# Kernel tuning notes

Hardware: AMD Instinct MI355X
Metric: run time of the kernel (lower is better)

Reference implementation:

```python
import jax, jax.numpy as jnp
import numpy as np

B, L, D, H = 2, 2048, 1024, 16
DH = D // H  # 64


def setup_inputs() -> dict:
    key = jax.random.key(0)
    ks = jax.random.split(key, 9)
    s = 1.0 / np.sqrt(D)
    x = jax.random.normal(ks[0], (B, L, D), dtype=jnp.float32)
    # per-head projection weights stacked on leading head axis (torch Linear: y = x W^T + b)
    Wq = jax.random.normal(ks[1], (H, D, DH), dtype=jnp.float32) * s
    bq = jax.random.normal(ks[2], (H, DH), dtype=jnp.float32) * s
    Wk = jax.random.normal(ks[3], (H, D, DH), dtype=jnp.float32) * s
    bk = jax.random.normal(ks[4], (H, DH), dtype=jnp.float32) * s
    Wv = jax.random.normal(ks[5], (H, D, DH), dtype=jnp.float32) * s
    bv = jax.random.normal(ks[6], (H, DH), dtype=jnp.float32) * s
    WO = jax.random.normal(ks[7], (D, D), dtype=jnp.float32) * s  # torch layout [out, in]
    bO = jax.random.normal(ks[8], (D,), dtype=jnp.float32) * s
    return {"x": x, "Wq": Wq, "bq": bq, "Wk": Wk, "bk": bk,
            "Wv": Wv, "bv": bv, "WO": WO, "bO": bO}


def reference(x, Wq, bq, Wk, bk, Wv, bv, WO, bO):
    # Q,K,V: [B,H,L,DH]
    Q = jnp.einsum('bld,hdk->bhlk', x, Wq) + bq[None, :, None, :]
    K = jnp.einsum('bld,hdk->bhlk', x, Wk) + bk[None, :, None, :]
    V = jnp.einsum('bld,hdk->bhlk', x, Wv) + bv[None, :, None, :]
    scale = 1.0 / jnp.sqrt(jnp.asarray(DH, dtype=x.dtype))
    att = jnp.einsum('bhik,bhjk->bhij', Q, K) * scale  # [B,H,Lq,Lk]
    # NOTE: original softmaxes over dim=1 of [B,Lq,Lk] -> the QUERY axis (axis=2 here)
    att = jax.nn.softmax(att, axis=2)
    # dropout is identity in eval/reference mode
    out = jnp.einsum('bhij,bhjk->bhik', att, V)  # [B,H,L,DH]
    out = out.transpose(0, 2, 1, 3).reshape(B, L, D)  # concat heads on feature axis
    return jnp.einsum('bld,ed->ble', out, WO) + bO
```

## Files before the change

### kernel.cpp

```cpp
#include <hip/hip_runtime.h>
#include <math.h>

#define NB 2
#define NL 2048
#define ND 1024
#define NH 16
#define NDH 64
static constexpr float SCALE = 0.125f;

typedef short          bhalf8 __attribute__((ext_vector_type(8)));
typedef unsigned short ush8   __attribute__((ext_vector_type(8)));
typedef unsigned short ush4   __attribute__((ext_vector_type(4)));
typedef float          f32x4  __attribute__((ext_vector_type(4)));

#define MFMA_BF16(a, b, c) __builtin_amdgcn_mfma_f32_16x16x32_bf16(a, b, c, 0, 0, 0)

__device__ __forceinline__ unsigned short f2bf(float f) {
    unsigned u = __float_as_uint(f);
    u += 0x7FFF + ((u >> 16) & 1);
    return (unsigned short)(u >> 16);
}
__device__ __forceinline__ float bf2f(unsigned short s) {
    return __uint_as_float((unsigned)s << 16);
}
__device__ __forceinline__ unsigned pack_bf16(float lo, float hi) {
    unsigned a = __float_as_uint(lo) + 0x8000u;
    unsigned b = __float_as_uint(hi) + 0x8000u;
    return __builtin_amdgcn_perm(b, a, 0x07060302u);
}

__global__ __launch_bounds__(256) void k_cvt(
    const float* __restrict__ x, const float* __restrict__ WO,
    unsigned short* __restrict__ xb, unsigned short* __restrict__ wob)
{
    size_t u = (size_t)blockIdx.x * 256 + threadIdx.x;
    const float* src; unsigned short* dst; size_t off;
    if (u < 524288) { src = x;  dst = xb;  off = u * 8; }
    else            { src = WO; dst = wob; off = (u - 524288) * 8; }
    float4 a = *(const float4*)(src + off);
    float4 b = *(const float4*)(src + off + 4);
    uint4 o;
    o.x = pack_bf16(a.x, a.y); o.y = pack_bf16(a.z, a.w);
    o.z = pack_bf16(b.x, b.y); o.w = pack_bf16(b.z, b.w);
    *(uint4*)(dst + off) = o;
}

__global__ __launch_bounds__(256) void k_cvt_wt(
    const float* __restrict__ Wq, const float* __restrict__ Wk,
    const float* __restrict__ Wv, unsigned short* __restrict__ Wtb)
{
    __shared__ unsigned short T[64][72];
    const int d0  = blockIdx.x * 64;
    const int qkv = blockIdx.y >> 4;
    const int h   = blockIdx.y & 15;
    const float* W = (qkv == 0 ? Wq : (qkv == 1 ? Wk : Wv)) + (size_t)h * (ND * NDH);
    const int t = threadIdx.x;
#pragma unroll
    for (int p = 0; p < 4; ++p) {
        int u  = t + p * 256;
        int dr = u >> 4;
        int c4 = (u & 15) * 4;
        float4 v = *(const float4*)(W + (size_t)(d0 + dr) * NDH + c4);
        T[c4 + 0][dr] = f2bf(v.x);
        T[c4 + 1][dr] = f2bf(v.y);
        T[c4 + 2][dr] = f2bf(v.z);
        T[c4 + 3][dr] = f2bf(v.w);
    }
    __syncthreads();
    unsigned short* outp = Wtb + (size_t)(qkv * NH + h) * NDH * ND;
#pragma unroll
    for (int p = 0; p < 2; ++p) {
        int u  = t + p * 256;
        int dh = u >> 3;
        int sg = (u & 7) * 8;
        *(ush8*)(outp + (size_t)dh * ND + d0 + sg) = *(ush8*)&T[dh][sg];
    }
}

__global__ __launch_bounds__(256, 2) void k_qkv_mfma(
    const unsigned short* __restrict__ xb, const unsigned short* __restrict__ Wtb,
    const float* __restrict__ bq, const float* __restrict__ bk,
    const float* __restrict__ bv,
    unsigned short* __restrict__ Qb, unsigned short* __restrict__ Kb,
    unsigned short* __restrict__ Vtb)
{
    __shared__ unsigned short LB[2 * 128 * 64];
    unsigned short* As = LB;
    unsigned short* Bs = LB + 128 * 64;

    const int mt = blockIdx.x;
    const int nt = blockIdx.y;
    const int qkv = nt >> 3;
    const int t = threadIdx.x, w = t >> 6, lane = t & 63;
    const int lr = lane & 15, lg = lane >> 4;
    const int wm = (w >> 1) * 64, wn = (w & 1) * 64;
    const int swz = (lr & 7) << 3;

    f32x4 acc[4][4] = {};

    for (int k0 = 0; k0 < ND; k0 += 64) {
        __syncthreads();
#pragma unroll
        for (int p = 0; p < 4; ++p) {
            int u = t + p * 256;
            int r = u >> 3, sg = (u & 7) * 8;
            int sc = sg ^ ((r & 7) << 3);
            *(ush8*)&As[r * 64 + sc] = *(const ush8*)(xb  + (size_t)(mt * 128 + r) * ND + k0 + sg);
            *(ush8*)&Bs[r * 64 + sc] = *(const ush8*)(Wtb + (size_t)(nt * 128 + r) * ND + k0 + sg);
        }
        __syncthreads();

        bhalf8 av[4][2], bw[4][2];
#pragma unroll
        for (int f = 0; f < 4; ++f)
#pragma unroll
            for (int ks = 0; ks < 2; ++ks) {
                int c = (ks * 32 + lg * 8) ^ swz;
                av[f][ks] = *(const bhalf8*)&As[(wm + f * 16 + lr) * 64 + c];
                bw[f][ks] = *(const bhalf8*)&Bs[(wn + f * 16 + lr) * 64 + c];
            }
#pragma unroll
        for (int mf = 0; mf < 4; ++mf)
#pragma unroll
            for (int nf = 0; nf < 4; ++nf) {
                acc[mf][nf] = MFMA_BF16(av[mf][0], bw[nf][0], acc[mf][nf]);
                acc[mf][nf] = MFMA_BF16(av[mf][1], bw[nf][1], acc[mf][nf]);
            }
    }

    const float* bias = (qkv == 0 ? bq : (qkv == 1 ? bk : bv));
    const int nb = (nt & 7) * 128;
    float bi[4];
#pragma unroll
    for (int nf = 0; nf < 4; ++nf) bi[nf] = bias[nb + wn + nf * 16 + lr];

    __syncthreads();
    unsigned short* TS = LB;

    if (qkv < 2) {
#pragma unroll
        for (int mf = 0; mf < 4; ++mf)
#pragma unroll
            for (int nf = 0; nf < 4; ++nf)
#pragma unroll
                for (int r = 0; r < 4; ++r) {
                    int m = wm + mf * 16 + lg * 4 + r;
                    int n = (wn + nf * 16 + lr) ^ ((m & 7) << 3);
                    TS[m * 128 + n] = f2bf(acc[mf][nf][r] + bi[nf]);
                }
        __syncthreads();
        unsigned short* outp = (qkv == 0 ? Qb : Kb);
#pragma unroll
        for (int p = 0; p < 8; ++p) {
            int u = t + p * 256;
            int r = u >> 4, sg = (u & 15) * 8;
            ush8 v = *(const ush8*)&TS[r * 128 + (sg ^ ((r & 7) << 3))];
            int m = mt * 128 + r;
            int b = m >> 11, l = m & (NL - 1);
            int n = nb + sg;
            int h = n >> 6, dh = n & 63;
            *(ush8*)(outp + ((size_t)(b * NH + h) * NL + l) * NDH + dh) = v;
        }
    } else {
#pragma unroll
        for (int mf = 0; mf < 4; ++mf)
#pragma unroll
            for (int nf = 0; nf < 4; ++nf) {
                int n = wn + nf * 16 + lr;
                int mc = (wm + mf * 16 + lg * 4) ^ ((n & 7) << 3);
                ush4 pk;
#pragma unroll
                for (int r = 0; r < 4; ++r) pk[r] = f2bf(acc[mf][nf][r] + bi[nf]);
                *(ush4*)&TS[n * 128 + mc] = pk;
            }
        __syncthreads();
#pragma unroll
        for (int p = 0; p < 8; ++p) {
            int u = t + p * 256;
            int r = u >> 4, sg = (u & 15) * 8;
            ush8 v = *(const ush8*)&TS[r * 128 + (sg ^ ((r & 7) << 3))];
            int n = nb + r;
            int h = n >> 6, dh = n & 63;
            int m0 = mt * 128 + sg;
            int b = m0 >> 11, l0 = m0 & (NL - 1);
            *(ush8*)(Vtb + ((size_t)(b * NH + h) * NDH + dh) * NL + l0) = v;
        }
    }
}

__global__ __launch_bounds__(256, 3) void k_colsum_mfma(
    const unsigned short* __restrict__ Qb, const unsigned short* __restrict__ Kb,
    unsigned short* __restrict__ Vtb)
{
    __shared__ unsigned short Ks[128 * 64];
    __shared__ unsigned short Qs[64 * 64];
    __shared__ float rzbuf[128];

    const int jt = blockIdx.x;
    const int bh = blockIdx.y;
    const unsigned short* Qp = Qb + (size_t)bh * NL * NDH;
    const unsigned short* Kp = Kb + (size_t)bh * NL * NDH;
    const int t = threadIdx.x, w = t >> 6, lane = t & 63;
    const int lr = lane & 15, lg = lane >> 4;
    const int wj = w * 32;
    const int swz = (lr & 7) << 3;

#pragma unroll
    for (int p = 0; p < 4; ++p) {
        int u = t + p * 256;
        int r = u >> 3, sg = (u & 7) * 8;
        *(ush8*)&Ks[r * 64 + (sg ^ ((r & 7) << 3))] =
            *(const ush8*)(Kp + (size_t)(jt * 128 + r) * NDH + sg);
    }

    float zacc[2][4] = {};

    for (int it = 0; it < 32; ++it) {
        __syncthreads();
#pragma unroll
        for (int p = 0; p < 2; ++p) {
            int u = t + p * 256;
            int r = u >> 3, sg = (u & 7) * 8;
            *(ush8*)&Qs[r * 64 + (sg ^ ((r & 7) << 3))] =
                *(const ush8*)(Qp + (size_t)(it * 64 + r) * NDH + sg);
        }
        __syncthreads();

        bhalf8 ka[2][2], qv[4][2];
#pragma unroll
        for (int jf = 0; jf < 2; ++jf)
#pragma unroll
            for (int ks = 0; ks < 2; ++ks)
                ka[jf][ks] = *(const bhalf8*)&Ks[(wj + jf * 16 + lr) * 64 +
                                                ((ks * 32 + lg * 8) ^ swz)];
#pragma unroll
        for (int ii = 0; ii < 4; ++ii)
#pragma unroll
            for (int ks = 0; ks < 2; ++ks)
                qv[ii][ks] = *(const bhalf8*)&Qs[(ii * 16 + lr) * 64 +
                                                ((ks * 32 + lg * 8) ^ swz)];

#pragma unroll
        for (int jf = 0; jf < 2; ++jf)
#pragma unroll
            for (int ii = 0; ii < 4; ++ii) {
                f32x4 s = {};
                s = MFMA_BF16(ka[jf][0], qv[ii][0], s);
                s = MFMA_BF16(ka[jf][1], qv[ii][1], s);
#pragma unroll
                for (int r = 0; r < 4; ++r)
                    zacc[jf][r] += __expf(s[r] * SCALE);
            }
    }

#pragma unroll
    for (int jf = 0; jf < 2; ++jf)
#pragma unroll
        for (int r = 0; r < 4; ++r) {
            float v = zacc[jf][r];
            v += __shfl_xor(v, 1);
            v += __shfl_xor(v, 2);
            v += __shfl_xor(v, 4);
            v += __shfl_xor(v, 8);
            zacc[jf][r] = v;
        }
    if (lr == 0) {
#pragma unroll
        for (int jf = 0; jf < 2; ++jf)
#pragma unroll
            for (int r = 0; r < 4; ++r)
                rzbuf[wj + jf * 16 + lg * 4 + r] = 1.0f / zacc[jf][r];
    }
    __syncthreads();

    unsigned short* Vp = Vtb + (size_t)bh * NDH * NL + jt * 128;
#pragma unroll
    for (int p = 0; p < 4; ++p) {
        int u = t + p * 256;
        int dh = u >> 4, jj = (u & 15) * 8;
        unsigned short* vp = Vp + (size_t)dh * NL + jj;
        ush8 v = *(const ush8*)vp;
        float4 z0 = *(const float4*)&rzbuf[jj];
        float4 z1 = *(const float4*)&rzbuf[jj + 4];
        uint4 o;
        o.x = pack_bf16(bf2f(v[0]) * z0.x, bf2f(v[1]) * z0.y);
        o.y = pack_bf16(bf2f(v[2]) * z0.z, bf2f(v[3]) * z0.w);
        o.z = pack_bf16(bf2f(v[4]) * z1.x, bf2f(v[5]) * z1.y);
        o.w = pack_bf16(bf2f(v[6]) * z1.z, bf2f(v[7]) * z1.w);
        *(uint4*)vp = o;
    }
}

__global__ __launch_bounds__(256, 3) void k_av_mfma(
    const unsigned short* __restrict__ Qb, const unsigned short* __restrict__ Kb,
    const unsigned short* __restrict__ Vtb, unsigned short* __restrict__ AOb)
{
    __shared__ unsigned short Qs[128 * 64];
    __shared__ unsigned short Ks[64 * 64];
    __shared__ unsigned short Vts[64 * 64];
    __shared__ unsigned short Ps[128 * 64];

    const int it = blockIdx.x;
    const int bh = blockIdx.y;
    const int b = bh >> 4, h = bh & 15;
    const unsigned short* Qp = Qb  + (size_t)bh * NL * NDH;
    const unsigned short* Kp = Kb  + (size_t)bh * NL * NDH;
    const unsigned short* Vp = Vtb + (size_t)bh * NDH * NL;

    const int t = threadIdx.x, w = t >> 6, lane = t & 63;
    const int lr = lane & 15, lg = lane >> 4;
    const int wi = w * 32;
    const int swz = (lr & 7) << 3;

#pragma unroll
    for (int p = 0; p < 4; ++p) {
        int u = t + p * 256;
        int r = u >> 3, sg = (u & 7) * 8;
        *(ush8*)&Qs[r * 64 + (sg ^ ((r & 7) << 3))] =
            *(const ush8*)(Qp + (size_t)(it * 128 + r) * NDH + sg);
    }

    f32x4 oacc[2][4] = {};

    for (int jt = 0; jt < 32; ++jt) {
        __syncthreads();
#pragma unroll
        for (int p = 0; p < 2; ++p) {
            int u = t + p * 256;
            int r = u >> 3, sg = (u & 7) * 8;
            int sc = sg ^ ((r & 7) << 3);
            *(ush8*)&Ks[r * 64 + sc]  = *(const ush8*)(Kp + (size_t)(jt * 64 + r) * NDH + sg);
            *(ush8*)&Vts[r * 64 + sc] = *(const ush8*)(Vp + (size_t)r * NL + jt * 64 + sg);
        }
        __syncthreads();

        bhalf8 ka[4][2], qv[2][2];
#pragma unroll
        for (int jf = 0; jf < 4; ++jf)
#pragma unroll
            for (int ks = 0; ks < 2; ++ks)
                ka[jf][ks] = *(const bhalf8*)&Ks[(jf * 16 + lr) * 64 +
                                                ((ks * 32 + lg * 8) ^ swz)];
#pragma unroll
        for (int ii = 0; ii < 2; ++ii)
#pragma unroll
            for (int ks = 0; ks < 2; ++ks)
                qv[ii][ks] = *(const bhalf8*)&Qs[(wi + ii * 16 + lr) * 64 +
                                                ((ks * 32 + lg * 8) ^ swz)];

#pragma unroll
        for (int ii = 0; ii < 2; ++ii)
#pragma unroll
            for (int jf = 0; jf < 4; ++jf) {
                f32x4 s = {};
                s = MFMA_BF16(ka[jf][0], qv[ii][0], s);
                s = MFMA_BF16(ka[jf][1], qv[ii][1], s);
                uint2 pk;
                pk.x = pack_bf16(__expf(s[0] * SCALE), __expf(s[1] * SCALE));
                pk.y = pack_bf16(__expf(s[2] * SCALE), __expf(s[3] * SCALE));
                *(uint2*)&Ps[(wi + ii * 16 + lr) * 64 + ((jf * 16 + lg * 4) ^ swz)] = pk;
            }
        __syncthreads();

        bhalf8 pa[2][2], vb[4][2];
#pragma unroll
        for (int ii = 0; ii < 2; ++ii)
#pragma unroll
            for (int ks = 0; ks < 2; ++ks)
                pa[ii][ks] = *(const bhalf8*)&Ps[(wi + ii * 16 + lr) * 64 +
                                                ((ks * 32 + lg * 8) ^ swz)];
#pragma unroll
        for (int nf = 0; nf < 4; ++nf)
#pragma unroll
            for (int ks = 0; ks < 2; ++ks)
                vb[nf][ks] = *(const bhalf8*)&Vts[(nf * 16 + lr) * 64 +
                                                 ((ks * 32 + lg * 8) ^ swz)];
#pragma unroll
        for (int ii = 0; ii < 2; ++ii)
#pragma unroll
            for (int nf = 0; nf < 4; ++nf) {
                oacc[ii][nf] = MFMA_BF16(pa[ii][0], vb[nf][0], oacc[ii][nf]);
                oacc[ii][nf] = MFMA_BF16(pa[ii][1], vb[nf][1], oacc[ii][nf]);
            }
    }

    __syncthreads();
#pragma unroll
    for (int ii = 0; ii < 2; ++ii)
#pragma unroll
        for (int nf = 0; nf < 4; ++nf)
#pragma unroll
            for (int r = 0; r < 4; ++r) {
                int l  = wi + ii * 16 + lg * 4 + r;
                int dh = (nf * 16 + lr) ^ ((l & 7) << 3);
                Ps[l * 64 + dh] = f2bf(oacc[ii][nf][r]);
            }
    __syncthreads();
#pragma unroll
    for (int p = 0; p < 4; ++p) {
        int u = t + p * 256;
        int r = u >> 3, sg = (u & 7) * 8;
        ush8 v = *(const ush8*)&Ps[r * 64 + (sg ^ ((r & 7) << 3))];
        *(ush8*)(AOb + ((size_t)(b * NL + it * 128 + r)) * ND + h * NDH + sg) = v;
    }
}

__global__ __launch_bounds__(256, 2) void k_oproj_mfma(
    const unsigned short* __restrict__ AOb, const unsigned short* __restrict__ WOb,
    const float* __restrict__ bO, float* __restrict__ y)
{
    __shared__ unsigned short As[128 * 64];
    __shared__ unsigned short Bs[128 * 64];

    const int mt = blockIdx.x;
    const int nt = blockIdx.y;
    const int t = threadIdx.x, w = t >> 6, lane = t & 63;
    const int lr = lane & 15, lg = lane >> 4;
    const int wm = (w >> 1) * 64, wn = (w & 1) * 64;
    const int swz = (lr & 7) << 3;

    f32x4 acc[4][4] = {};

    for (int k0 = 0; k0 < ND; k0 += 64) {
        __syncthreads();
#pragma unroll
        for (int p = 0; p < 4; ++p) {
            int u = t + p * 256;
            int r = u >> 3, sg = (u & 7) * 8;
            int sc = sg ^ ((r & 7) << 3);
            *(ush8*)&As[r * 64 + sc] = *(const ush8*)(AOb + (size_t)(mt * 128 + r) * ND + k0 + sg);
            *(ush8*)&Bs[r * 64 + sc] = *(const ush8*)(WOb + (size_t)(nt * 128 + r) * ND + k0 + sg);
        }
        __syncthreads();

        bhalf8 av[4][2], bw[4][2];
#pragma unroll
        for (int f = 0; f < 4; ++f)
#pragma unroll
            for (int ks = 0; ks < 2; ++ks) {
                int c = (ks * 32 + lg * 8) ^ swz;
                av[f][ks] = *(const bhalf8*)&As[(wm + f * 16 + lr) * 64 + c];
                bw[f][ks] = *(const bhalf8*)&Bs[(wn + f * 16 + lr) * 64 + c];
            }
#pragma unroll
        for (int mf = 0; mf < 4; ++mf)
#pragma unroll
            for (int nf = 0; nf < 4; ++nf) {
                acc[mf][nf] = MFMA_BF16(av[mf][0], bw[nf][0], acc[mf][nf]);
                acc[mf][nf] = MFMA_BF16(av[mf][1], bw[nf][1], acc[mf][nf]);
            }
    }

#pragma unroll
    for (int mf = 0; mf < 4; ++mf)
#pragma unroll
        for (int nf = 0; nf < 4; ++nf) {
            int e = nt * 128 + wn + nf * 16 + lr;
            float bo = bO[e];
#pragma unroll
            for (int r = 0; r < 4; ++r) {
                int m = mt * 128 + wm + mf * 16 + lg * 4 + r;
                y[(size_t)m * ND + e] = acc[mf][nf][r] + bo;
            }
        }
}

extern "C" void kernel_launch(void* const* d_in, const int* in_sizes, int n_in,
                              void* d_out, int out_size, void* d_ws, size_t ws_size,
                              hipStream_t stream)
{
    const float* x  = (const float*)d_in[0];
    const float* Wq = (const float*)d_in[1];
    const float* bq = (const float*)d_in[2];
    const float* Wk = (const float*)d_in[3];
    const float* bk = (const float*)d_in[4];
    const float* Wv = (const float*)d_in[5];
    const float* bv = (const float*)d_in[6];
    const float* WO = (const float*)d_in[7];
    const float* bO = (const float*)d_in[8];
    float* y = (float*)d_out;

    unsigned short* xb  = (unsigned short*)d_ws;
    unsigned short* Wtb = xb  + 4194304;
    unsigned short* WOb = Wtb + 3145728;
    unsigned short* Qb  = WOb + 1048576;
    unsigned short* Kb  = Qb  + 4194304;
    unsigned short* Vtb = Kb  + 4194304;
    unsigned short* AOb = Vtb + 4194304;

    hipLaunchKernelGGL(k_cvt,         dim3(2560),   dim3(256), 0, stream, x, WO, xb, WOb);
    hipLaunchKernelGGL(k_cvt_wt,      dim3(16, 48), dim3(256), 0, stream, Wq, Wk, Wv, Wtb);
    hipLaunchKernelGGL(k_qkv_mfma,    dim3(32, 24), dim3(256), 0, stream,
                       xb, Wtb, bq, bk, bv, Qb, Kb, Vtb);
    hipLaunchKernelGGL(k_colsum_mfma, dim3(16, 32), dim3(256), 0, stream, Qb, Kb, Vtb);
    hipLaunchKernelGGL(k_av_mfma,     dim3(16, 32), dim3(256), 0, stream, Qb, Kb, Vtb, AOb);
    hipLaunchKernelGGL(k_oproj_mfma,  dim3(32, 8),  dim3(256), 0, stream, AOb, WOb, bO, y);
}
```

Measured before the change: 231.8 us.

## Use direct global-to-LDS loads, 512-thread attention blocks, smaller o-proj tiles

Global-to-shared tile staging in the QKV, column-sum, attention and output-projection kernels now uses `global_load_lds` 16-byte DMA loads. The swizzle is applied on the global source address, so data no longer passes through registers. The column-sum and A·V kernels move to 512-thread blocks, giving each wave a single 16-row slice and fewer registers, which should raise occupancy and latency hiding. The output projection uses 64-row M tiles, doubling the grid to fill more CUs, at the cost of less B-tile reuse per block.

After: 215.7 us. 1.07x faster.

```diff
diff --git a/kernel.cpp b/kernel.cpp
--- a/kernel.cpp
+++ b/kernel.cpp
@@ -27,6 +27,12 @@
     unsigned a = __float_as_uint(lo) + 0x8000u;
     unsigned b = __float_as_uint(hi) + 0x8000u;
     return __builtin_amdgcn_perm(b, a, 0x07060302u);
+}
+__device__ __forceinline__ void gload16(const unsigned short* g, unsigned short* l) {
+    __builtin_amdgcn_global_load_lds(
+        (const __attribute__((address_space(1))) unsigned int*)(const void*)g,
+        (__attribute__((address_space(3))) unsigned int*)(void*)l,
+        16, 0, 0);
 }
 
 __global__ __launch_bounds__(256) void k_cvt(
@@ -95,18 +101,19 @@
     const int lr = lane & 15, lg = lane >> 4;
     const int wm = (w >> 1) * 64, wn = (w & 1) * 64;
     const int swz = (lr & 7) << 3;
+    const int rA = lane >> 3, cg = (lane & 7) * 8;
 
     f32x4 acc[4][4] = {};
 
     for (int k0 = 0; k0 < ND; k0 += 64) {
         __syncthreads();
 #pragma unroll
-        for (int p = 0; p < 4; ++p) {
-            int u = t + p * 256;
-            int r = u >> 3, sg = (u & 7) * 8;
-            int sc = sg ^ ((r & 7) << 3);
-            *(ush8*)&As[r * 64 + sc] = *(const ush8*)(xb  + (size_t)(mt * 128 + r) * ND + k0 + sg);
-            *(ush8*)&Bs[r * 64 + sc] = *(const ush8*)(Wtb + (size_t)(nt * 128 + r) * ND + k0 + sg);
+        for (int i = 0; i < 4; ++i) {
+            int c  = w * 4 + i;
+            int r  = c * 8 + rA;
+            int gc = cg ^ ((r & 7) << 3);
+            gload16(xb  + (size_t)(mt * 128 + r) * ND + k0 + gc, &As[c * 512]);
+            gload16(Wtb + (size_t)(nt * 128 + r) * ND + k0 + gc, &Bs[c * 512]);
         }
         __syncthreads();
 
@@ -188,7 +195,7 @@
     }
 }
 
-__global__ __launch_bounds__(256, 3) void k_colsum_mfma(
+__global__ __launch_bounds__(512, 4) void k_colsum_mfma(
     const unsigned short* __restrict__ Qb, const unsigned short* __restrict__ Kb,
     unsigned short* __restrict__ Vtb)
 {
@@ -202,96 +209,81 @@
     const unsigned short* Kp = Kb + (size_t)bh * NL * NDH;
     const int t = threadIdx.x, w = t >> 6, lane = t & 63;
     const int lr = lane & 15, lg = lane >> 4;
-    const int wj = w * 32;
+    const int wj = w * 16;
     const int swz = (lr & 7) << 3;
-
-#pragma unroll
-    for (int p = 0; p < 4; ++p) {
-        int u = t + p * 256;
-        int r = u >> 3, sg = (u & 7) * 8;
-        *(ush8*)&Ks[r * 64 + (sg ^ ((r & 7) << 3))] =
-            *(const ush8*)(Kp + (size_t)(jt * 128 + r) * NDH + sg);
-    }
-
-    float zacc[2][4] = {};
+    const int rA = lane >> 3, cg = (lane & 7) * 8;
+
+#pragma unroll
+    for (int i = 0; i < 2; ++i) {
+        int c  = w * 2 + i;
+        int r  = c * 8 + rA;
+        int gc = cg ^ ((r & 7) << 3);
+        gload16(Kp + (size_t)(jt * 128 + r) * NDH + gc, &Ks[c * 512]);
+    }
+
+    float zacc[4] = {};
 
     for (int it = 0; it < 32; ++it) {
         __syncthreads();
-#pragma unroll
-        for (int p = 0; p < 2; ++p) {
-            int u = t + p * 256;
-            int r = u >> 3, sg = (u & 7) * 8;
-            *(ush8*)&Qs[r * 64 + (sg ^ ((r & 7) << 3))] =
-                *(const ush8*)(Qp + (size_t)(it * 64 + r) * NDH + sg);
-        }
-        __syncthreads();
-
-        bhalf8 ka[2][2], qv[4][2];
-#pragma unroll
-        for (int jf = 0; jf < 2; ++jf)
-#pragma unroll
-            for (int ks = 0; ks < 2; ++ks)
-                ka[jf][ks] = *(const bhalf8*)&Ks[(wj + jf * 16 + lr) * 64 +
-                                                ((ks * 32 + lg * 8) ^ swz)];
-#pragma unroll
-        for (int ii = 0; ii < 4; ++ii)
-#pragma unroll
-            for (int ks = 0; ks < 2; ++ks)
-                qv[ii][ks] = *(const bhalf8*)&Qs[(ii * 16 + lr) * 64 +
-                                                ((ks * 32 + lg * 8) ^ swz)];
-
-#pragma unroll
-        for (int jf = 0; jf < 2; ++jf)
-#pragma unroll
-            for (int ii = 0; ii < 4; ++ii) {
-                f32x4 s = {};
-                s = MFMA_BF16(ka[jf][0], qv[ii][0], s);
-                s = MFMA_BF16(ka[jf][1], qv[ii][1], s);
-#pragma unroll
-                for (int r = 0; r < 4; ++r)
-                    zacc[jf][r] += __expf(s[r] * SCALE);
-            }
-    }
-
-#pragma unroll
-    for (int jf = 0; jf < 2; ++jf)
-#pragma unroll
-        for (int r = 0; r < 4; ++r) {
-            float v = zacc[jf][r];
-            v += __shfl_xor(v, 1);
-            v += __shfl_xor(v, 2);
-            v += __shfl_xor(v, 4);
-            v += __shfl_xor(v, 8);
-            zacc[jf][r] = v;
-        }
-    if (lr == 0) {
-#pragma unroll
-        for (int jf = 0; jf < 2; ++jf)
-#pragma unroll
-            for (int r = 0; r < 4; ++r)
-                rzbuf[wj + jf * 16 + lg * 4 + r] = 1.0f / zacc[jf][r];
+        {
+            int r  = w * 8 + rA;
+            int gc = cg ^ ((r & 7) << 3);
+            gload16(Qp + (size_t)(it * 64 + r) * NDH + gc, &Qs[w * 512]);
+        }
+        __syncthreads();
+
+        bhalf8 ka[2];
+#pragma unroll
+        for (int ks = 0; ks < 2; ++ks)
+            ka[ks] = *(const bhalf8*)&Ks[(wj + lr) * 64 + ((ks * 32 + lg * 8) ^ swz)];
+#pragma unroll
+        for (int ii = 0; ii < 4; ++ii) {
+            bhalf8 q0 = *(const bhalf8*)&Qs[(ii * 16 + lr) * 64 + ((lg * 8) ^ swz)];
+            bhalf8 q1 = *(const bhalf8*)&Qs[(ii * 16 + lr) * 64 + ((32 + lg * 8) ^ swz)];
+            f32x4 s = {};
+            s = MFMA_BF16(ka[0], q0, s);
+            s = MFMA_BF16(ka[1], q1, s);
+#pragma unroll
+            for (int r = 0; r < 4; ++r) zacc[r] += __expf(s[r] * SCALE);
+        }
+    }
+
+#pragma unroll
+    for (int r = 0; r < 4; ++r) {
+        float v = zacc[r];
+        v += __shfl_xor(v, 1);
+        v += __shfl_xor(v, 2);
+        v += __shfl_xor(v, 4);
+        v += __shfl_xor(v, 8);
+        if (lr == 0) rzbuf[wj + lg * 4 + r] = 1.0f / v;
     }
     __syncthreads();
 
     unsigned short* Vp = Vtb + (size_t)bh * NDH * NL + jt * 128;
-#pragma unroll
-    for (int p = 0; p < 4; ++p) {
-        int u = t + p * 256;
-        int dh = u >> 4, jj = (u & 15) * 8;
+    {
+        int dh = t >> 3, jj = (t & 7) * 16;
         unsigned short* vp = Vp + (size_t)dh * NL + jj;
-        ush8 v = *(const ush8*)vp;
+        ush8 v0 = *(const ush8*)vp;
+        ush8 v1 = *(const ush8*)(vp + 8);
         float4 z0 = *(const float4*)&rzbuf[jj];
         float4 z1 = *(const float4*)&rzbuf[jj + 4];
-        uint4 o;
-        o.x = pack_bf16(bf2f(v[0]) * z0.x, bf2f(v[1]) * z0.y);
-        o.y = pack_bf16(bf2f(v[2]) * z0.z, bf2f(v[3]) * z0.w);
-        o.z = pack_bf16(bf2f(v[4]) * z1.x, bf2f(v[5]) * z1.y);
-        o.w = pack_bf16(bf2f(v[6]) * z1.z, bf2f(v[7]) * z1.w);
-        *(uint4*)vp = o;
-    }
-}
-
-__global__ __launch_bounds__(256, 3) void k_av_mfma(
+        float4 z2 = *(const float4*)&rzbuf[jj + 8];
+        float4 z3 = *(const float4*)&rzbuf[jj + 12];
+        uint4 o0, o1;
+        o0.x = pack_bf16(bf2f(v0[0]) * z0.x, bf2f(v0[1]) * z0.y);
+        o0.y = pack_bf16(bf2f(v0[2]) * z0.z, bf2f(v0[3]) * z0.w);
+        o0.z = pack_bf16(bf2f(v0[4]) * z1.x, bf2f(v0[5]) * z1.y);
+        o0.w = pack_bf16(bf2f(v0[6]) * z1.z, bf2f(v0[7]) * z1.w);
+        o1.x = pack_bf16(bf2f(v1[0]) * z2.x, bf2f(v1[1]) * z2.y);
+        o1.y = pack_bf16(bf2f(v1[2]) * z2.z, bf2f(v1[3]) * z2.w);
+        o1.z = pack_bf16(bf2f(v1[4]) * z3.x, bf2f(v1[5]) * z3.y);
+        o1.w = pack_bf16(bf2f(v1[6]) * z3.z, bf2f(v1[7]) * z3.w);
+        *(uint4*)vp = o0;
+        *(uint4*)(vp + 8) = o1;
+    }
+}
+
+__global__ __launch_bounds__(512, 4) void k_av_mfma(
     const unsigned short* __restrict__ Qb, const unsigned short* __restrict__ Kb,
     const unsigned short* __restrict__ Vtb, unsigned short* __restrict__ AOb)
 {
@@ -309,99 +301,78 @@
 
     const int t = threadIdx.x, w = t >> 6, lane = t & 63;
     const int lr = lane & 15, lg = lane >> 4;
-    const int wi = w * 32;
+    const int wi = w * 16;
     const int swz = (lr & 7) << 3;
-
-#pragma unroll
-    for (int p = 0; p < 4; ++p) {
-        int u = t + p * 256;
-        int r = u >> 3, sg = (u & 7) * 8;
-        *(ush8*)&Qs[r * 64 + (sg ^ ((r & 7) << 3))] =
-            *(const ush8*)(Qp + (size_t)(it * 128 + r) * NDH + sg);
-    }
-
-    f32x4 oacc[2][4] = {};
+    const int rA = lane >> 3, cg = (lane & 7) * 8;
+
+#pragma unroll
+    for (int i = 0; i < 2; ++i) {
+        int c  = w * 2 + i;
+        int r  = c * 8 + rA;
+        int gc = cg ^ ((r & 7) << 3);
+        gload16(Qp + (size_t)(it * 128 + r) * NDH + gc, &Qs[c * 512]);
+    }
+
+    f32x4 oacc[4] = {};
 
     for (int jt = 0; jt < 32; ++jt) {
         __syncthreads();
-#pragma unroll
-        for (int p = 0; p < 2; ++p) {
-            int u = t + p * 256;
-            int r = u >> 3, sg = (u & 7) * 8;
-            int sc = sg ^ ((r & 7) << 3);
-            *(ush8*)&Ks[r * 64 + sc]  = *(const ush8*)(Kp + (size_t)(jt * 64 + r) * NDH + sg);
-            *(ush8*)&Vts[r * 64 + sc] = *(const ush8*)(Vp + (size_t)r * NL + jt * 64 + sg);
-        }
-        __syncthreads();
-
-        bhalf8 ka[4][2], qv[2][2];
-#pragma unroll
-        for (int jf = 0; jf < 4; ++jf)
-#pragma unroll
-            for (int ks = 0; ks < 2; ++ks)
-                ka[jf][ks] = *(const bhalf8*)&Ks[(jf * 16 + lr) * 64 +
-                                                ((ks * 32 + lg * 8) ^ swz)];
-#pragma unroll
-        for (int ii = 0; ii < 2; ++ii)
-#pragma unroll
-            for (int ks = 0; ks < 2; ++ks)
-                qv[ii][ks] = *(const bhalf8*)&Qs[(wi + ii * 16 + lr) * 64 +
-                                                ((ks * 32 + lg * 8) ^ swz)];
-
-#pragma unroll
-        for (int ii = 0; ii < 2; ++ii)
-#pragma unroll
-            for (int jf = 0; jf < 4; ++jf) {
-                f32x4 s = {};
-                s = MFMA_BF16(ka[jf][0], qv[ii][0], s);
-                s = MFMA_BF16(ka[jf][1], qv[ii][1], s);
-                uint2 pk;
-                pk.x = pack_bf16(__expf(s[0] * SCALE), __expf(s[1] * SCALE));
-                pk.y = pack_bf16(__expf(s[2] * SCALE), __expf(s[3] * SCALE));
-                *(uint2*)&Ps[(wi + ii * 16 + lr) * 64 + ((jf * 16 + lg * 4) ^ swz)] = pk;
-            }
-        __syncthreads();
-
-        bhalf8 pa[2][2], vb[4][2];
-#pragma unroll
-        for (int ii = 0; ii < 2; ++ii)
-#pragma unroll
-            for (int ks = 0; ks < 2; ++ks)
-                pa[ii][ks] = *(const bhalf8*)&Ps[(wi + ii * 16 + lr) * 64 +
-                                                ((ks * 32 + lg * 8) ^ swz)];
-#pragma unroll
-        for (int nf = 0; nf < 4; ++nf)
-#pragma unroll
-            for (int ks = 0; ks < 2; ++ks)
-                vb[nf][ks] = *(const bhalf8*)&Vts[(nf * 16 + lr) * 64 +
-                                                 ((ks * 32 + lg * 8) ^ swz)];
-#pragma unroll
-        for (int ii = 0; ii < 2; ++ii)
-#pragma unroll
-            for (int nf = 0; nf < 4; ++nf) {
-                oacc[ii][nf] = MFMA_BF16(pa[ii][0], vb[nf][0], oacc[ii][nf]);
-                oacc[ii][nf] = MFMA_BF16(pa[ii][1], vb[nf][1], oacc[ii][nf]);
-            }
+        {
+            int r  = w * 8 + rA;
+            int gc = cg ^ ((r & 7) << 3);
+            gload16(Kp + (size_t)(jt * 64 + r) * NDH + gc, &Ks[w * 512]);
+            gload16(Vp + (size_t)r * NL + jt * 64 + gc,    &Vts[w * 512]);
+        }
+        __syncthreads();
+
+        bhalf8 qa[2];
+#pragma unroll
+        for (int ks = 0; ks < 2; ++ks)
+            qa[ks] = *(const bhalf8*)&Qs[(wi + lr) * 64 + ((ks * 32 + lg * 8) ^ swz)];
+#pragma unroll
+        for (int jf = 0; jf < 4; ++jf) {
+            bhalf8 k0v = *(const bhalf8*)&Ks[(jf * 16 + lr) * 64 + ((lg * 8) ^ swz)];
+            bhalf8 k1v = *(const bhalf8*)&Ks[(jf * 16 + lr) * 64 + ((32 + lg * 8) ^ swz)];
+            f32x4 s = {};
+            s = MFMA_BF16(k0v, qa[0], s);
+            s = MFMA_BF16(k1v, qa[1], s);
+            uint2 pk;
+            pk.x = pack_bf16(__expf(s[0] * SCALE), __expf(s[1] * SCALE));
+            pk.y = pack_bf16(__expf(s[2] * SCALE), __expf(s[3] * SCALE));
+            *(uint2*)&Ps[(wi + lr) * 64 + ((jf * 16 + lg * 4) ^ swz)] = pk;
+        }
+
+        bhalf8 pa[2];
+#pragma unroll
+        for (int ks = 0; ks < 2; ++ks)
+            pa[ks] = *(const bhalf8*)&Ps[(wi + lr) * 64 + ((ks * 32 + lg * 8) ^ swz)];
+#pragma unroll
+        for (int nf = 0; nf < 4; ++nf) {
+            bhalf8 v0 = *(const bhalf8*)&Vts[(nf * 16 + lr) * 64 + ((lg * 8) ^ swz)];
+            bhalf8 v1 = *(const bhalf8*)&Vts[(nf * 16 + lr) * 64 + ((32 + lg * 8) ^ swz)];
+            oacc[nf] = MFMA_BF16(pa[0], v0, oacc[nf]);
+            oacc[nf] = MFMA_BF16(pa[1], v1, oacc[nf]);
+        }
     }
 
     __syncthreads();
 #pragma unroll
-    for (int ii = 0; ii < 2; ++ii)
-#pragma unroll
-        for (int nf = 0; nf < 4; ++nf)
-#pragma unroll
-            for (int r = 0; r < 4; ++r) {
-                int l  = wi + ii * 16 + lg * 4 + r;
-                int dh = (nf * 16 + lr) ^ ((l & 7) << 3);
-                Ps[l * 64 + dh] = f2bf(oacc[ii][nf][r]);
-            }
+    for (int nf = 0; nf < 4; ++nf)
+#pragma unroll
+        for (int r = 0; r < 4; ++r) {
+            int li  = wi + lg * 4 + r;
+            int dhc = (nf * 16 + lr) ^ ((li & 7) << 3);
+            Ps[li * 64 + dhc] = f2bf(oacc[nf][r]);
+        }
     __syncthreads();
-#pragma unroll
-    for (int p = 0; p < 4; ++p) {
-        int u = t + p * 256;
-        int r = u >> 3, sg = (u & 7) * 8;
-        ush8 v = *(const ush8*)&Ps[r * 64 + (sg ^ ((r & 7) << 3))];
-        *(ush8*)(AOb + ((size_t)(b * NL + it * 128 + r)) * ND + h * NDH + sg) = v;
+    {
+        int r = t >> 2, sgq = (t & 3) * 16;
+        int sz2 = (r & 7) << 3;
+        ush8 v0 = *(const ush8*)&Ps[r * 64 + (sgq ^ sz2)];
+        ush8 v1 = *(const ush8*)&Ps[r * 64 + ((sgq + 8) ^ sz2)];
+        unsigned short* op = AOb + ((size_t)(b * NL + it * 128 + r)) * ND + h * NDH + sgq;
+        *(ush8*)op = v0;
+        *(ush8*)(op + 8) = v1;
     }
 }
 
@@ -409,57 +380,65 @@
     const unsigned short* __restrict__ AOb, const unsigned short* __restrict__ WOb,
     const float* __restrict__ bO, float* __restrict__ y)
 {
-    __shared__ unsigned short As[128 * 64];
+    __shared__ unsigned short As[64 * 64];
     __shared__ unsigned short Bs[128 * 64];
 
     const int mt = blockIdx.x;
     const int nt = blockIdx.y;
     const int t = threadIdx.x, w = t >> 6, lane = t & 63;
     const int lr = lane & 15, lg = lane >> 4;
-    const int wm = (w >> 1) * 64, wn = (w & 1) * 64;
+    const int wn = w * 32;
     const int swz = (lr & 7) << 3;
-
-    f32x4 acc[4][4] = {};
+    const int rA = lane >> 3, cg = (lane & 7) * 8;
+
+    f32x4 acc[4][2] = {};
 
     for (int k0 = 0; k0 < ND; k0 += 64) {
         __syncthreads();
 #pragma unroll
-        for (int p = 0; p < 4; ++p) {
-            int u = t + p * 256;
-            int r = u >> 3, sg = (u & 7) * 8;
-            int sc = sg ^ ((r & 7) << 3);
-            *(ush8*)&As[r * 64 + sc] = *(const ush8*)(AOb + (size_t)(mt * 128 + r) * ND + k0 + sg);
-            *(ush8*)&Bs[r * 64 + sc] = *(const ush8*)(WOb + (size_t)(nt * 128 + r) * ND + k0 + sg);
-        }
-        __syncthreads();
-
-        bhalf8 av[4][2], bw[4][2];
-#pragma unroll
-        for (int f = 0; f < 4; ++f)
-#pragma unroll
-            for (int ks = 0; ks < 2; ++ks) {
-                int c = (ks * 32 + lg * 8) ^ swz;
-                av[f][ks] = *(const bhalf8*)&As[(wm + f * 16 + lr) * 64 + c];
-                bw[f][ks] = *(const bhalf8*)&Bs[(wn + f * 16 + lr) * 64 + c];
+        for (int i = 0; i < 2; ++i) {
+            int c  = w * 2 + i;
+            int r  = c * 8 + rA;
+            int gc = cg ^ ((r & 7) << 3);
+            gload16(AOb + (size_t)(mt * 64 + r) * ND + k0 + gc, &As[c * 512]);
+        }
+#pragma unroll
+        for (int i = 0; i < 4; ++i) {
+            int c  = w * 4 + i;
+            int r  = c * 8 + rA;
+            int gc = cg ^ ((r & 7) << 3);
+            gload16(WOb + (size_t)(nt * 128 + r) * ND + k0 + gc, &Bs[c * 512]);
+        }
+        __syncthreads();
+
+        bhalf8 bw[2][2];
+#pragma unroll
+        for (int nf = 0; nf < 2; ++nf)
+#pragma unroll
+            for (int ks = 0; ks < 2; ++ks)
+                bw[nf][ks] = *(const bhalf8*)&Bs[(wn + nf * 16 + lr) * 64 +
+                                                ((ks * 32 + lg * 8) ^ swz)];
+#pragma unroll
+        for (int mf = 0; mf < 4; ++mf) {
+            bhalf8 a0 = *(const bhalf8*)&As[(mf * 16 + lr) * 64 + ((lg * 8) ^ swz)];
+            bhalf8 a1 = *(const bhalf8*)&As[(mf * 16 + lr) * 64 + ((32 + lg * 8) ^ swz)];
+#pragma unroll
+            for (int nf = 0; nf < 2; ++nf) {
+                acc[mf][nf] = MFMA_BF16(a0, bw[nf][0], acc[mf][nf]);
+                acc[mf][nf] = MFMA_BF16(a1, bw[nf][1], acc[mf][nf]);
             }
-#pragma unroll
-        for (int mf = 0; mf < 4; ++mf)
-#pragma unroll
-            for (int nf = 0; nf < 4; ++nf) {
-                acc[mf][nf] = MFMA_BF16(av[mf][0], bw[nf][0], acc[mf][nf]);
-                acc[mf][nf] = MFMA_BF16(av[mf][1], bw[nf][1], acc[mf][nf]);
-            }
+        }
     }
 
 #pragma unroll
     for (int mf = 0; mf < 4; ++mf)
 #pragma unroll
-        for (int nf = 0; nf < 4; ++nf) {
+        for (int nf = 0; nf < 2; ++nf) {
             int e = nt * 128 + wn + nf * 16 + lr;
             float bo = bO[e];
 #pragma unroll
             for (int r = 0; r < 4; ++r) {
-                int m = mt * 128 + wm + mf * 16 + lg * 4 + r;
+                int m = mt * 64 + mf * 16 + lg * 4 + r;
                 y[(size_t)m * ND + e] = acc[mf][nf][r] + bo;
             }
         }
@@ -492,7 +471,7 @@
     hipLaunchKernelGGL(k_cvt_wt,      dim3(16, 48), dim3(256), 0, stream, Wq, Wk, Wv, Wtb);
     hipLaunchKernelGGL(k_qkv_mfma,    dim3(32, 24), dim3(256), 0, stream,
                        xb, Wtb, bq, bk, bv, Qb, Kb, Vtb);
-    hipLaunchKernelGGL(k_colsum_mfma, dim3(16, 32), dim3(256), 0, stream, Qb, Kb, Vtb);
-    hipLaunchKernelGGL(k_av_mfma,     dim3(16, 32), dim3(256), 0, stream, Qb, Kb, Vtb, AOb);
-    hipLaunchKernelGGL(k_oproj_mfma,  dim3(32, 8),  dim3(256), 0, stream, AOb, WOb, bO, y);
-}
+    hipLaunchKernelGGL(k_colsum_mfma, dim3(16, 32), dim3(512), 0, stream, Qb, Kb, Vtb);
+    hipLaunchKernelGGL(k_av_mfma,     dim3(16, 32), dim3(512), 0, stream, Qb, Kb, Vtb, AOb);
+    hipLaunchKernelGGL(k_oproj_mfma,  dim3(64, 8),  dim3(256), 0, stream, AOb, WOb, bO, y);
+}
```
